# Performance work log

Hardware: AMD Instinct MI355X
Metric: run time of the kernel (lower is better)

The kernel has to match this reference:

```python
import jax, jax.numpy as jnp
import numpy as np

N = 1_000_000   # total cluster nodes
D = 128         # input_dim
B = 4096        # number of scenes (segments)
M = 1024        # rows in dist embeddings


def setup_inputs() -> dict:
    key = jax.random.key(0)
    ks = jax.random.split(key, 16)
    inp = {
        "x_clu": jax.random.normal(ks[0], (N, D), dtype=jnp.float32),
        "mask_clu": jax.random.bernoulli(ks[1], 0.9, (N,)),
        "batch_clu": jnp.sort(jax.random.randint(ks[2], (N,), 0, B, dtype=jnp.int32)),
        "dist_embedding": jax.random.normal(ks[3], (M, 6), dtype=jnp.float32),
        "dist_embedding_norm": jax.random.normal(ks[4], (M, 1), dtype=jnp.float32),
        # AttentionalAggregation gate: Linear(D, 1)
        "gate_w": jax.random.normal(ks[5], (D, 1), dtype=jnp.float32) / np.sqrt(D),
        "gate_b": jnp.zeros((1,), dtype=jnp.float32),
        # vel_si_vec MLP [D, D, 6]
        "w1": jax.random.normal(ks[6], (D, D), dtype=jnp.float32) / np.sqrt(D),
        "b1": jnp.zeros((D,), dtype=jnp.float32),
        "w2": jax.random.normal(ks[7], (D, 6), dtype=jnp.float32) / np.sqrt(D),
        "b2": jnp.zeros((6,), dtype=jnp.float32),
        # vel_si_norm MLP [D, D, 1]
        "w1n": jax.random.normal(ks[8], (D, D), dtype=jnp.float32) / np.sqrt(D),
        "b1n": jnp.zeros((D,), dtype=jnp.float32),
        "w2n": jax.random.normal(ks[9], (D, 1), dtype=jnp.float32) / np.sqrt(D),
        "b2n": jnp.zeros((1,), dtype=jnp.float32),
    }
    return inp


def _attn_pool(x, mask, seg, gate_w, gate_b):
    # gate logits for every node; masked nodes excluded from the segment softmax
    gate = jnp.einsum("nd,do->n", x, gate_w) + gate_b[0]           # [N]
    neg = jnp.finfo(gate.dtype).min
    gate = jnp.where(mask, gate, neg)
    gmax = jax.ops.segment_max(gate, seg, num_segments=B)          # [B]
    e = jnp.where(mask, jnp.exp(gate - gmax[seg]), 0.0)            # [N]
    denom = jax.ops.segment_sum(e, seg, num_segments=B)            # [B]
    w = e / jnp.maximum(denom[seg], 1e-12)                         # [N]
    return jax.ops.segment_sum(w[:, None] * x, seg, num_segments=B)  # [B, D]


def reference(x_clu, mask_clu, batch_clu, dist_embedding, dist_embedding_norm,
              gate_w, gate_b, w1, b1, w2, b2, w1n, b1n, w2n, b2n):
    x_scene = _attn_pool(x_clu, mask_clu, batch_clu, gate_w, gate_b)  # [B, D]
    vel = jax.nn.relu(x_scene @ w1 + b1) @ w2 + b2                    # [B, 6]
    nrm = jax.nn.relu(x_scene @ w1n + b1n) @ w2n + b2n                # [B, 1]
    out_vec = vel * jnp.mean(dist_embedding, axis=0)                  # [B, 6]
    out_norm = nrm * jnp.mean(dist_embedding_norm, axis=0)            # [B, 1]
    return out_vec, out_norm
```

## Files before the change

kernel.cpp:

```cpp
#include <hip/hip_runtime.h>

#define D 128

__global__ void means_kernel(const float* __restrict__ de, const float* __restrict__ den,
                             int M, float* __restrict__ out7) {
    __shared__ float sm[256][8];
    float a[7];
#pragma unroll
    for (int j = 0; j < 7; ++j) a[j] = 0.f;
    for (int r = threadIdx.x; r < M; r += 256) {
#pragma unroll
        for (int j = 0; j < 6; ++j) a[j] += de[r * 6 + j];
        a[6] += den[r];
    }
#pragma unroll
    for (int j = 0; j < 7; ++j) sm[threadIdx.x][j] = a[j];
    __syncthreads();
    for (int s = 128; s > 0; s >>= 1) {
        if (threadIdx.x < (unsigned)s) {
#pragma unroll
            for (int j = 0; j < 7; ++j) sm[threadIdx.x][j] += sm[threadIdx.x + s][j];
        }
        __syncthreads();
    }
    if (threadIdx.x < 7) out7[threadIdx.x] = sm[0][threadIdx.x] / (float)M;
}

__global__ void bounds_kernel(const int* __restrict__ seg, int N, int B,
                              int* __restrict__ off) {
    int i = blockIdx.x * blockDim.x + threadIdx.x;
    if (i > N) return;
    int cur  = (i < N) ? seg[i]     : B;
    int prev = (i > 0) ? seg[i - 1] : -1;
    for (int j = prev + 1; j <= cur; ++j) off[j] = i;
}

__global__ void stream_kernel(const float* __restrict__ x, const int* __restrict__ mask,
                              const int* __restrict__ off,
                              const float* __restrict__ gate_w, const float* __restrict__ gate_b,
                              float* __restrict__ partials) {
    const int b    = blockIdx.x >> 1;
    const int h    = blockIdx.x & 1;
    const int tid  = threadIdx.x;
    const int wv   = tid >> 6;
    const int lane = tid & 63;
    const int q    = lane >> 4;
    const int l16  = lane & 15;
    const int part = (wv << 2) | q;

    const int start = off[b];
    const int end   = off[b + 1];

    const float4 gwA = ((const float4*)gate_w)[l16];
    const float4 gwB = ((const float4*)gate_w)[16 + l16];
    const float  gb  = gate_b[0];

    float  s    = 0.f;
    float4 accA = {0.f, 0.f, 0.f, 0.f};
    float4 accB = {0.f, 0.f, 0.f, 0.f};
    const int last = end - 1;

#pragma unroll 4
    for (int i = start + (h << 4); i < end; i += 32) {
        const int row = i + (wv << 2) + q;
        const int r   = min(row, last);
        const float* xr = x + (size_t)r * D;
        const float4 xa = ((const float4*)xr)[l16];
        const float4 xb = ((const float4*)xr)[16 + l16];
        const int    mk = mask[r];
        float p = xa.x * gwA.x + xa.y * gwA.y + xa.z * gwA.z + xa.w * gwA.w
                + xb.x * gwB.x + xb.y * gwB.y + xb.z * gwB.z + xb.w * gwB.w;
#pragma unroll
        for (int o = 8; o > 0; o >>= 1) p += __shfl_xor(p, o);
        const float e = (row < end && mk != 0) ? __expf(p + gb) : 0.f;
        s      += e;
        accA.x += e * xa.x; accA.y += e * xa.y; accA.z += e * xa.z; accA.w += e * xa.w;
        accB.x += e * xb.x; accB.y += e * xb.y; accB.z += e * xb.z; accB.w += e * xb.w;
    }

    __shared__ float sacc[16][D + 4];
    __shared__ float ss[16];
    *(float4*)&sacc[part][l16 * 4]      = accA;
    *(float4*)&sacc[part][64 + l16 * 4] = accB;
    if (l16 == 0) ss[part] = s;
    __syncthreads();

    float* outp = partials + (size_t)blockIdx.x * 132;
    if (tid < D) {
        float A = 0.f;
#pragma unroll
        for (int k = 0; k < 16; ++k) A += sacc[k][tid];
        outp[tid] = A;
    } else if (tid == D) {
        float S = 0.f;
#pragma unroll
        for (int k = 0; k < 16; ++k) S += ss[k];
        outp[D] = S;
    }
}

__global__ void combine_mlp_kernel(const float* __restrict__ partials,
                                   const float* __restrict__ w1, const float* __restrict__ b1,
                                   const float* __restrict__ w2, const float* __restrict__ b2,
                                   const float* __restrict__ w1n, const float* __restrict__ b1n,
                                   const float* __restrict__ w2n, const float* __restrict__ b2n,
                                   const float* __restrict__ means,
                                   float* __restrict__ out_vec, float* __restrict__ out_norm) {
    const int b   = blockIdx.x;
    const int tid = threadIdx.x;
    const float* p0 = partials + (size_t)(2 * b) * 132;
    const float* p1 = p0 + 132;

    __shared__ float xs[D];
    if (tid < D) {
        const float S = fmaxf(p0[D] + p1[D], 1e-12f);
        xs[tid] = (p0[tid] + p1[tid]) / S;
    }
    __syncthreads();

    __shared__ float hid[D], hidn[D];
    if (tid < D) {
        float a1 = b1[tid];
#pragma unroll 8
        for (int i = 0; i < D; ++i) a1 += xs[i] * w1[i * D + tid];
        hid[tid] = fmaxf(a1, 0.f);
    } else {
        const int hh = tid - D;
        float a1n = b1n[hh];
#pragma unroll 8
        for (int i = 0; i < D; ++i) a1n += xs[i] * w1n[i * D + hh];
        hidn[hh] = fmaxf(a1n, 0.f);
    }
    __syncthreads();

    if (tid < 112) {
        const int g = tid >> 4, l = tid & 15;
        float o = 0.f;
        if (g < 6) {
#pragma unroll
            for (int k = 0; k < 8; ++k) { const int i = l * 8 + k; o += hid[i] * w2[i * 6 + g]; }
        } else {
#pragma unroll
            for (int k = 0; k < 8; ++k) { const int i = l * 8 + k; o += hidn[i] * w2n[i]; }
        }
#pragma unroll
        for (int of = 8; of > 0; of >>= 1) o += __shfl_xor(o, of);
        if (l == 0) {
            if (g < 6) out_vec[b * 6 + g] = (o + b2[g]) * means[g];
            else       out_norm[b]        = (o + b2n[0]) * means[6];
        }
    }
}

extern "C" void kernel_launch(void* const* d_in, const int* in_sizes, int n_in,
                              void* d_out, int out_size, void* d_ws, size_t ws_size,
                              hipStream_t stream) {
    const float* x      = (const float*)d_in[0];
    const int*   mask   = (const int*)  d_in[1];
    const int*   seg    = (const int*)  d_in[2];
    const float* de     = (const float*)d_in[3];
    const float* den    = (const float*)d_in[4];
    const float* gate_w = (const float*)d_in[5];
    const float* gate_b = (const float*)d_in[6];
    const float* w1     = (const float*)d_in[7];
    const float* b1     = (const float*)d_in[8];
    const float* w2     = (const float*)d_in[9];
    const float* b2     = (const float*)d_in[10];
    const float* w1n    = (const float*)d_in[11];
    const float* b1n    = (const float*)d_in[12];
    const float* w2n    = (const float*)d_in[13];
    const float* b2n    = (const float*)d_in[14];

    const int N  = in_sizes[1];
    const int M  = in_sizes[4];
    const int Bn = out_size / 7;

    float* means    = (float*)d_ws;
    int*   off      = (int*)d_ws + 16;
    float* partials = (float*)d_ws + 8192;
    float* out_vec  = (float*)d_out;
    float* out_norm = (float*)d_out + (size_t)Bn * 6;

    means_kernel<<<1, 256, 0, stream>>>(de, den, M, means);
    bounds_kernel<<<(N + 256) / 256, 256, 0, stream>>>(seg, N, Bn, off);
    stream_kernel<<<2 * Bn, 256, 0, stream>>>(x, mask, off, gate_w, gate_b, partials);
    combine_mlp_kernel<<<Bn, 256, 0, stream>>>(partials, w1, b1, w2, b2,
                                               w1n, b1n, w2n, b2n, means,
                                               out_vec, out_norm);
}
```

Before: 708.6 us.

## Split rows evenly across waves with segment-boundary atomics instead of per-segment blocks

Replaces the per-segment block decomposition, and the bounds kernel that built segment offsets, with a flat even split of rows across 8192 waves. Each wave walks its own row range, handles segment changes by reducing lanes and flushing with atomicAdd into zeroed per-segment partials, and software-prefetches the next row group. The means computation and the zeroing of the partials are merged into one prep kernel, which saves a launch. This aims to fix load imbalance and the launch overhead of the bounds pass, at the cost of float atomics (nondeterministic summation order) and a data-dependent inner loop at segment boundaries.

Result: no change. 713.5 us (+0.7%).

```diff
diff --git a/kernel.cpp b/kernel.cpp
--- a/kernel.cpp
+++ b/kernel.cpp
@@ -1,120 +1,160 @@
 #include <hip/hip_runtime.h>
 
 #define D 128
-
-__global__ void means_kernel(const float* __restrict__ de, const float* __restrict__ den,
-                             int M, float* __restrict__ out7) {
-    __shared__ float sm[256][8];
-    float a[7];
-#pragma unroll
-    for (int j = 0; j < 7; ++j) a[j] = 0.f;
-    for (int r = threadIdx.x; r < M; r += 256) {
-#pragma unroll
-        for (int j = 0; j < 6; ++j) a[j] += de[r * 6 + j];
-        a[6] += den[r];
-    }
-#pragma unroll
-    for (int j = 0; j < 7; ++j) sm[threadIdx.x][j] = a[j];
-    __syncthreads();
-    for (int s = 128; s > 0; s >>= 1) {
-        if (threadIdx.x < (unsigned)s) {
-#pragma unroll
-            for (int j = 0; j < 7; ++j) sm[threadIdx.x][j] += sm[threadIdx.x + s][j];
-        }
+#define PSTRIDE 132
+
+__global__ __launch_bounds__(256) void prep_kernel(
+        const float* __restrict__ de, const float* __restrict__ den, int M,
+        float* __restrict__ means, float* __restrict__ partials, int nPartF4) {
+    if (blockIdx.x == 0) {
+        __shared__ float sm[256][8];
+        float a[7];
+#pragma unroll
+        for (int j = 0; j < 7; ++j) a[j] = 0.f;
+        for (int r = threadIdx.x; r < M; r += 256) {
+#pragma unroll
+            for (int j = 0; j < 6; ++j) a[j] += de[r * 6 + j];
+            a[6] += den[r];
+        }
+#pragma unroll
+        for (int j = 0; j < 7; ++j) sm[threadIdx.x][j] = a[j];
         __syncthreads();
-    }
-    if (threadIdx.x < 7) out7[threadIdx.x] = sm[0][threadIdx.x] / (float)M;
-}
-
-__global__ void bounds_kernel(const int* __restrict__ seg, int N, int B,
-                              int* __restrict__ off) {
-    int i = blockIdx.x * blockDim.x + threadIdx.x;
-    if (i > N) return;
-    int cur  = (i < N) ? seg[i]     : B;
-    int prev = (i > 0) ? seg[i - 1] : -1;
-    for (int j = prev + 1; j <= cur; ++j) off[j] = i;
-}
-
-__global__ void stream_kernel(const float* __restrict__ x, const int* __restrict__ mask,
-                              const int* __restrict__ off,
-                              const float* __restrict__ gate_w, const float* __restrict__ gate_b,
-                              float* __restrict__ partials) {
-    const int b    = blockIdx.x >> 1;
-    const int h    = blockIdx.x & 1;
+        for (int s = 128; s > 0; s >>= 1) {
+            if (threadIdx.x < (unsigned)s) {
+#pragma unroll
+                for (int j = 0; j < 7; ++j) sm[threadIdx.x][j] += sm[threadIdx.x + s][j];
+            }
+            __syncthreads();
+        }
+        if (threadIdx.x < 7) means[threadIdx.x] = sm[0][threadIdx.x] / (float)M;
+    } else {
+        const int i = (blockIdx.x - 1) * 256 + threadIdx.x;
+        if (i < nPartF4) ((float4*)partials)[i] = make_float4(0.f, 0.f, 0.f, 0.f);
+    }
+}
+
+__global__ __launch_bounds__(256) void stream_kernel(
+        const float* __restrict__ x, const int* __restrict__ mask,
+        const int* __restrict__ seg, int N, int rowsPerWave,
+        const float* __restrict__ gate_w, const float* __restrict__ gate_b,
+        float* __restrict__ partials) {
     const int tid  = threadIdx.x;
     const int wv   = tid >> 6;
     const int lane = tid & 63;
     const int q    = lane >> 4;
     const int l16  = lane & 15;
-    const int part = (wv << 2) | q;
-
-    const int start = off[b];
-    const int end   = off[b + 1];
+
+    const int gwave = blockIdx.x * 4 + wv;
+    const int i0 = gwave * rowsPerWave;
+    const int i1 = min(i0 + rowsPerWave, N);
+    if (i0 >= i1) return;
+    const int last = i1 - 1;
 
     const float4 gwA = ((const float4*)gate_w)[l16];
     const float4 gwB = ((const float4*)gate_w)[16 + l16];
     const float  gb  = gate_b[0];
 
+    int    cur  = seg[i0];
     float  s    = 0.f;
     float4 accA = {0.f, 0.f, 0.f, 0.f};
     float4 accB = {0.f, 0.f, 0.f, 0.f};
-    const int last = end - 1;
-
-#pragma unroll 4
-    for (int i = start + (h << 4); i < end; i += 32) {
-        const int row = i + (wv << 2) + q;
-        const int r   = min(row, last);
-        const float* xr = x + (size_t)r * D;
-        const float4 xa = ((const float4*)xr)[l16];
-        const float4 xb = ((const float4*)xr)[16 + l16];
-        const int    mk = mask[r];
+
+    int r0 = min(i0 + q, last);
+    const float* xr0 = x + (size_t)r0 * D;
+    float4 xa = ((const float4*)xr0)[l16];
+    float4 xb = ((const float4*)xr0)[16 + l16];
+    int    mk = mask[r0];
+    int    sg = seg[r0];
+
+    for (int i = i0; i < i1; i += 4) {
+        const int rn = min(i + 4 + q, last);
+        const float* xrn = x + (size_t)rn * D;
+        const float4 na  = ((const float4*)xrn)[l16];
+        const float4 nb  = ((const float4*)xrn)[16 + l16];
+        const int    nmk = mask[rn];
+        const int    nsg = seg[rn];
+
         float p = xa.x * gwA.x + xa.y * gwA.y + xa.z * gwA.z + xa.w * gwA.w
                 + xb.x * gwB.x + xb.y * gwB.y + xb.z * gwB.z + xb.w * gwB.w;
 #pragma unroll
         for (int o = 8; o > 0; o >>= 1) p += __shfl_xor(p, o);
-        const float e = (row < end && mk != 0) ? __expf(p + gb) : 0.f;
-        s      += e;
-        accA.x += e * xa.x; accA.y += e * xa.y; accA.z += e * xa.z; accA.w += e * xa.w;
-        accB.x += e * xb.x; accB.y += e * xb.y; accB.z += e * xb.z; accB.w += e * xb.w;
-    }
-
-    __shared__ float sacc[16][D + 4];
-    __shared__ float ss[16];
-    *(float4*)&sacc[part][l16 * 4]      = accA;
-    *(float4*)&sacc[part][64 + l16 * 4] = accB;
-    if (l16 == 0) ss[part] = s;
-    __syncthreads();
-
-    float* outp = partials + (size_t)blockIdx.x * 132;
-    if (tid < D) {
-        float A = 0.f;
-#pragma unroll
-        for (int k = 0; k < 16; ++k) A += sacc[k][tid];
-        outp[tid] = A;
-    } else if (tid == D) {
-        float S = 0.f;
-#pragma unroll
-        for (int k = 0; k < 16; ++k) S += ss[k];
-        outp[D] = S;
-    }
-}
-
-__global__ void combine_mlp_kernel(const float* __restrict__ partials,
-                                   const float* __restrict__ w1, const float* __restrict__ b1,
-                                   const float* __restrict__ w2, const float* __restrict__ b2,
-                                   const float* __restrict__ w1n, const float* __restrict__ b1n,
-                                   const float* __restrict__ w2n, const float* __restrict__ b2n,
-                                   const float* __restrict__ means,
-                                   float* __restrict__ out_vec, float* __restrict__ out_norm) {
+        const bool rowok = (i + q < i1) && (mk != 0);
+
+        while (true) {
+            const float e = (rowok && sg == cur) ? __expf(p + gb) : 0.f;
+            s      += e;
+            accA.x += e * xa.x; accA.y += e * xa.y; accA.z += e * xa.z; accA.w += e * xa.w;
+            accB.x += e * xb.x; accB.y += e * xb.y; accB.z += e * xb.z; accB.w += e * xb.w;
+            const int sgmax = __shfl(sg, 63);
+            if (sgmax == cur) break;
+            {
+#define RED4(v) v += __shfl_xor(v, 16); v += __shfl_xor(v, 32);
+                RED4(accA.x) RED4(accA.y) RED4(accA.z) RED4(accA.w)
+                RED4(accB.x) RED4(accB.y) RED4(accB.z) RED4(accB.w)
+                RED4(s)
+#undef RED4
+                float* pb = partials + (size_t)cur * PSTRIDE;
+                if (lane < 16) {
+                    atomicAdd(pb + l16 * 4 + 0, accA.x);
+                    atomicAdd(pb + l16 * 4 + 1, accA.y);
+                    atomicAdd(pb + l16 * 4 + 2, accA.z);
+                    atomicAdd(pb + l16 * 4 + 3, accA.w);
+                    atomicAdd(pb + 64 + l16 * 4 + 0, accB.x);
+                    atomicAdd(pb + 64 + l16 * 4 + 1, accB.y);
+                    atomicAdd(pb + 64 + l16 * 4 + 2, accB.z);
+                    atomicAdd(pb + 64 + l16 * 4 + 3, accB.w);
+                }
+                if (lane == 0) atomicAdd(pb + 128, s);
+                s = 0.f;
+                accA = make_float4(0.f, 0.f, 0.f, 0.f);
+                accB = make_float4(0.f, 0.f, 0.f, 0.f);
+            }
+            int nx = (sg > cur) ? sg : 0x7fffffff;
+            nx = min(nx, __shfl_xor(nx, 16));
+            nx = min(nx, __shfl_xor(nx, 32));
+            cur = nx;
+        }
+
+        xa = na; xb = nb; mk = nmk; sg = nsg;
+    }
+
+    {
+#define RED4(v) v += __shfl_xor(v, 16); v += __shfl_xor(v, 32);
+        RED4(accA.x) RED4(accA.y) RED4(accA.z) RED4(accA.w)
+        RED4(accB.x) RED4(accB.y) RED4(accB.z) RED4(accB.w)
+        RED4(s)
+#undef RED4
+        float* pb = partials + (size_t)cur * PSTRIDE;
+        if (lane < 16) {
+            atomicAdd(pb + l16 * 4 + 0, accA.x);
+            atomicAdd(pb + l16 * 4 + 1, accA.y);
+            atomicAdd(pb + l16 * 4 + 2, accA.z);
+            atomicAdd(pb + l16 * 4 + 3, accA.w);
+            atomicAdd(pb + 64 + l16 * 4 + 0, accB.x);
+            atomicAdd(pb + 64 + l16 * 4 + 1, accB.y);
+            atomicAdd(pb + 64 + l16 * 4 + 2, accB.z);
+            atomicAdd(pb + 64 + l16 * 4 + 3, accB.w);
+        }
+        if (lane == 0) atomicAdd(pb + 128, s);
+    }
+}
+
+__global__ __launch_bounds__(256) void combine_mlp_kernel(
+        const float* __restrict__ partials,
+        const float* __restrict__ w1, const float* __restrict__ b1,
+        const float* __restrict__ w2, const float* __restrict__ b2,
+        const float* __restrict__ w1n, const float* __restrict__ b1n,
+        const float* __restrict__ w2n, const float* __restrict__ b2n,
+        const float* __restrict__ means,
+        float* __restrict__ out_vec, float* __restrict__ out_norm) {
     const int b   = blockIdx.x;
     const int tid = threadIdx.x;
-    const float* p0 = partials + (size_t)(2 * b) * 132;
-    const float* p1 = p0 + 132;
+    const float* pb = partials + (size_t)b * PSTRIDE;
 
     __shared__ float xs[D];
     if (tid < D) {
-        const float S = fmaxf(p0[D] + p1[D], 1e-12f);
-        xs[tid] = (p0[tid] + p1[tid]) / S;
+        const float S = fmaxf(pb[128], 1e-12f);
+        xs[tid] = pb[tid] / S;
     }
     __syncthreads();
 
@@ -176,14 +216,18 @@
     const int Bn = out_size / 7;
 
     float* means    = (float*)d_ws;
-    int*   off      = (int*)d_ws + 16;
-    float* partials = (float*)d_ws + 8192;
+    float* partials = (float*)d_ws + 256;
     float* out_vec  = (float*)d_out;
     float* out_norm = (float*)d_out + (size_t)Bn * 6;
 
-    means_kernel<<<1, 256, 0, stream>>>(de, den, M, means);
-    bounds_kernel<<<(N + 256) / 256, 256, 0, stream>>>(seg, N, Bn, off);
-    stream_kernel<<<2 * Bn, 256, 0, stream>>>(x, mask, off, gate_w, gate_b, partials);
+    const int nPartF4   = Bn * PSTRIDE / 4;
+    const int zeroBlks  = (nPartF4 + 255) / 256;
+    const int nBlocks   = 2048;
+    const int nWaves    = nBlocks * 4;
+    const int rpw       = (((N + nWaves - 1) / nWaves) + 3) & ~3;
+
+    prep_kernel<<<1 + zeroBlks, 256, 0, stream>>>(de, den, M, means, partials, nPartF4);
+    stream_kernel<<<nBlocks, 256, 0, stream>>>(x, mask, seg, N, rpw, gate_w, gate_b, partials);
     combine_mlp_kernel<<<Bn, 256, 0, stream>>>(partials, w1, b1, w2, b2,
                                                w1n, b1n, w2n, b2n, means,
                                                out_vec, out_norm);
```
